# Kernel optimization log

Hardware: AMD Instinct MI355X
Metric: run time of the kernel (lower is better)

Reference implementation:

```python
import jax, jax.numpy as jnp
import numpy as np

N, E1, E2, P, H = 4096, 131072, 131072, 65536, 128
ROLE_VOCAB, ROLE_DIM, IDX_VOCAB, IDX_DIM = 8, 16, 1024, 8


def _lin_init(key, fan_in, fan_out):
    k1, k2 = jax.random.split(key)
    bound = 1.0 / np.sqrt(fan_in)
    W = jax.random.uniform(k1, (fan_in, fan_out), jnp.float32, -bound, bound)
    b = jax.random.uniform(k2, (fan_out,), jnp.float32, -bound, bound)
    return W, b


def setup_inputs() -> dict:
    key = jax.random.key(0)
    ks = jax.random.split(key, 24)
    d = {}
    d["block_features"] = jax.random.normal(ks[0], (N, 16), jnp.float32)
    d["role_ids"] = jax.random.randint(ks[1], (N,), 0, ROLE_VOCAB)
    d["b2b_src"] = jax.random.randint(ks[2], (E1,), 0, N)
    d["b2b_dst"] = jax.random.randint(ks[3], (E1,), 0, N)
    d["b2b_w"] = jax.random.uniform(ks[4], (E1,), jnp.float32)
    d["p2b_pin"] = jax.random.randint(ks[5], (E2,), 0, P)
    d["p2b_block"] = jax.random.randint(ks[6], (E2,), 0, N)
    d["p2b_w"] = jax.random.uniform(ks[7], (E2,), jnp.float32)
    d["pins_pos"] = jax.random.normal(ks[8], (P, 2), jnp.float32)
    d["area_targets"] = jax.random.uniform(ks[9], (N,), jnp.float32)
    # parameters
    d["role_emb"] = jax.random.normal(ks[10], (ROLE_VOCAB, ROLE_DIM), jnp.float32)
    d["idx_emb"] = jax.random.normal(ks[11], (IDX_VOCAB, IDX_DIM), jnp.float32)
    d["in_W1"], d["in_b1"] = _lin_init(ks[12], 16 + IDX_DIM + ROLE_DIM, H)
    d["in_W2"], d["in_b2"] = _lin_init(ks[13], H, H)
    d["b2b_W1"], d["b2b_b1"] = _lin_init(ks[14], 2 * H + 1, H)
    d["b2b_W2"], d["b2b_b2"] = _lin_init(ks[15], H, H)
    d["p2b_W1"], d["p2b_b1"] = _lin_init(ks[16], H + 3, H)
    d["p2b_W2"], d["p2b_b2"] = _lin_init(ks[17], H, H)
    d["self_W"], d["self_b"] = _lin_init(ks[18], H, H)
    d["ln_g"] = jnp.ones((H,), jnp.float32)
    d["ln_b"] = jnp.zeros((H,), jnp.float32)
    d["gp_W1"], d["gp_b1"] = _lin_init(ks[19], 2 * H, H)
    d["gp_W2"], d["gp_b2"] = _lin_init(ks[20], H, H)
    return d


def _mlp2(x, W1, b1, W2, b2):
    return jax.nn.relu(x @ W1 + b1) @ W2 + b2


def _forward(block_features, role_ids, b2b_src, b2b_dst, b2b_w, p2b_pin, p2b_block,
             p2b_w, pins_pos, area_targets, role_emb, idx_emb, in_W1, in_b1, in_W2,
             in_b2, b2b_W1, b2b_b1, b2b_W2, b2b_b2, p2b_W1, p2b_b1, p2b_W2, p2b_b2,
             self_W, self_b, ln_g, ln_b, gp_W1, gp_b1, gp_W2, gp_b2):
    n = block_features.shape[0]
    role_e = role_emb[role_ids]                       # [N, role_dim]
    idx_e = idx_emb[jnp.arange(n) % IDX_VOCAB]        # [N, idx_dim]
    x = jnp.concatenate([block_features, role_e, idx_e], axis=-1)
    h = jax.nn.relu(_mlp2(x, in_W1, in_b1, in_W2, in_b2))  # input_proj ends in ReLU

    # --- b2b messages: two directed messages per undirected edge ---
    max_b2b = jax.lax.stop_gradient(jnp.maximum(jnp.max(jnp.abs(b2b_w)), 1.0))
    w = (b2b_w / max_b2b)[:, None]                    # [E1, 1]
    hi, hj = h[b2b_src], h[b2b_dst]                   # [E1, H]
    m_ij = _mlp2(jnp.concatenate([hi, hj, w], -1), b2b_W1, b2b_b1, b2b_W2, b2b_b2)
    m_ji = _mlp2(jnp.concatenate([hj, hi, w], -1), b2b_W1, b2b_b1, b2b_W2, b2b_b2)
    agg = jnp.zeros_like(h).at[b2b_src].add(m_ij).at[b2b_dst].add(m_ji)

    # --- p2b messages ---
    total_area = jnp.maximum(jnp.sum(area_targets), 1e-6)
    case_scale = jax.lax.stop_gradient(jnp.maximum(jnp.sqrt(total_area), 1e-6))
    max_p2b = jax.lax.stop_gradient(jnp.maximum(jnp.max(jnp.abs(p2b_w)), 1.0))
    pin_feats = jnp.concatenate(
        [pins_pos[p2b_pin] / case_scale, (p2b_w / max_p2b)[:, None]], axis=-1)  # [E2, 3]
    m_p = _mlp2(jnp.concatenate([h[p2b_block], pin_feats], -1),
                p2b_W1, p2b_b1, p2b_W2, p2b_b2)
    agg = agg.at[p2b_block].add(m_p)

    # --- combine + LayerNorm ---
    z = h @ self_W + self_b + agg
    mu = jnp.mean(z, axis=-1, keepdims=True)
    var = jnp.mean(jnp.square(z - mu), axis=-1, keepdims=True)
    block_embeddings = (z - mu) / jnp.sqrt(var + 1e-5) * ln_g + ln_b

    pooled = jnp.concatenate(
        [block_embeddings.mean(axis=0), block_embeddings.max(axis=0)], axis=-1)
    graph_embedding = _mlp2(pooled, gp_W1, gp_b1, gp_W2, gp_b2)
    return block_embeddings, graph_embedding


def reference(block_features, role_ids, b2b_src, b2b_dst, b2b_w, p2b_pin, p2b_block,
              p2b_w, pins_pos, area_targets, role_emb, idx_emb, in_W1, in_b1, in_W2,
              in_b2, b2b_W1, b2b_b1, b2b_W2, b2b_b2, p2b_W1, p2b_b1, p2b_W2, p2b_b2,
              self_W, self_b, ln_g, ln_b, gp_W1, gp_b1, gp_W2, gp_b2):
    block_embeddings, graph_embedding = _forward(
        block_features, role_ids, b2b_src, b2b_dst, b2b_w, p2b_pin, p2b_block,
        p2b_w, pins_pos, area_targets, role_emb, idx_emb, in_W1, in_b1, in_W2,
        in_b2, b2b_W1, b2b_b1, b2b_W2, b2b_b2, p2b_W1, p2b_b1, p2b_W2, p2b_b2,
        self_W, self_b, ln_g, ln_b, gp_W1, gp_b1, gp_W2, gp_b2)
    block_mask = jnp.ones((block_features.shape[0],), dtype=bool)
    return block_embeddings, graph_embedding, block_mask
```

## Files before the change

### kernel.cpp

```cpp
#include <hip/hip_runtime.h>
#include <hip/hip_bf16.h>

#define N_NODES 4096
#define HDIM    128
#define E1      131072
#define E2      131072
#define NMSG_B2B (2 * E1)
#define CAPB    192
#define CAPP    96

#define OFF_PSUM   8
#define OFF_PMAX   136
#define OFF_HB     264
#define OFF_P      (OFF_HB + 262144)
#define OFF_Q      (OFF_P + 524288)
#define OFF_R      (OFF_Q + 524288)
#define OFF_CP     (OFF_R + 524288)
#define OFF_B2H    (OFF_CP + 24576)
#define OFF_B2L    (OFF_B2H + 8192)
#define OFF_P2H    (OFF_B2L + 8192)
#define OFF_P2L    (OFF_P2H + 8192)
#define OFF_SWP    (OFF_P2L + 8192)
#define OFF_IW1    (OFF_SWP + 8192)
#define OFF_IW2    (OFF_IW1 + 4096)
#define OFF_WLAST  (OFF_IW2 + 8192)
#define OFF_PEXTRA (OFF_WLAST + 128)
#define OFF_CNTB   (OFF_PEXTRA + 384)
#define OFF_CNTP   (OFF_CNTB + 4096)
#define OFF_BKB    (OFF_CNTP + 4096)
#define OFF_BKP    (OFF_BKB + 2 * N_NODES * CAPB)
#define WS_FLOATS  (OFF_BKP + 2 * N_NODES * CAPP)

typedef short short8 __attribute__((ext_vector_type(8)));
typedef float f32x4 __attribute__((ext_vector_type(4)));

__device__ __forceinline__ unsigned short f2bf(float f) {
  union { float f; unsigned u; } v; v.f = f;
  unsigned r = v.u + 0x7fffu + ((v.u >> 16) & 1u);
  return (unsigned short)(r >> 16);
}
__device__ __forceinline__ float bf2f(unsigned short h) {
  return __uint_as_float((unsigned)h << 16);
}
__device__ __forceinline__ int il(int c) { return ((c & 63) << 1) | (c >> 6); }

__global__ __launch_bounds__(256) void setup_kernel(const float* __restrict__ b2bw,
                                                    const float* __restrict__ p2bw,
                                                    const float* __restrict__ area,
                                                    const float* __restrict__ bW1,
                                                    const float* __restrict__ bW2,
                                                    const float* __restrict__ pW1,
                                                    const float* __restrict__ pW2,
                                                    const float* __restrict__ sWm,
                                                    const float* __restrict__ iW1,
                                                    const float* __restrict__ iW2,
                                                    float* __restrict__ ws) {
  __shared__ float red[256];
  int b = blockIdx.x, t = threadIdx.x;
  if (b < 32) {
    float m = 0.f;
    for (int i = b * 256 + t; i < E1; i += 32 * 256) m = fmaxf(m, fabsf(b2bw[i]));
    red[t] = m; __syncthreads();
    for (int s = 128; s > 0; s >>= 1) { if (t < s) red[t] = fmaxf(red[t], red[t + s]); __syncthreads(); }
    if (t == 0) atomicMax((unsigned*)&ws[0], __float_as_uint(red[0]));
  } else if (b < 64) {
    float m = 0.f;
    for (int i = (b - 32) * 256 + t; i < E2; i += 32 * 256) m = fmaxf(m, fabsf(p2bw[i]));
    red[t] = m; __syncthreads();
    for (int s = 128; s > 0; s >>= 1) { if (t < s) red[t] = fmaxf(red[t], red[t + s]); __syncthreads(); }
    if (t == 0) atomicMax((unsigned*)&ws[1], __float_as_uint(red[0]));
  } else if (b < 96) {
    float s0 = 0.f;
    for (int i = (b - 64) * 256 + t; i < N_NODES; i += 32 * 256) s0 += area[i];
    red[t] = s0; __syncthreads();
    for (int s = 128; s > 0; s >>= 1) { if (t < s) red[t] += red[t + s]; __syncthreads(); }
    if (t == 0) atomicAdd(&ws[2], red[0]);
  } else if (b == 96) {
    if (t < HDIM) ((int*)ws)[OFF_PMAX + t] = 0x80000000;
  } else {
    unsigned short* Cp  = (unsigned short*)(ws + OFF_CP);
    unsigned short* B2h = (unsigned short*)(ws + OFF_B2H);
    unsigned short* B2l = (unsigned short*)(ws + OFF_B2L);
    unsigned short* P2h = (unsigned short*)(ws + OFF_P2H);
    unsigned short* P2l = (unsigned short*)(ws + OFF_P2L);
    unsigned short* Swp = (unsigned short*)(ws + OFF_SWP);
    unsigned short* I1p = (unsigned short*)(ws + OFF_IW1);
    unsigned short* I2p = (unsigned short*)(ws + OFF_IW2);
    float* wlast = ws + OFF_WLAST;
    float* pextra = ws + OFF_PEXTRA;
    const int total = 156160;
    for (int x = (b - 97) * 256 + t; x < total; x += 128 * 256) {
      if (x < 49152) {
        int j = x & 7, lane = (x >> 3) & 63, ks = (x >> 9) & 3, nc = x >> 11;
        int col = nc * 16 + (lane & 15), k = ks * 32 + (lane >> 4) * 8 + j;
        float v;
        if (col < 128)      v = bW1[k * 128 + col];
        else if (col < 256) v = bW1[(128 + k) * 128 + (col - 128)];
        else                v = pW1[k * 128 + (col - 256)];
        Cp[x] = f2bf(v);
      } else if (x < 114688) {
        int u = (x - 49152) & 16383, which = (x - 49152) >> 14;
        int j = u & 7, lane = (u >> 3) & 63, ks = (u >> 9) & 3, nt = u >> 11;
        int n = nt * 16 + (lane & 15), k = ks * 32 + (lane >> 4) * 8 + j;
        float v = (which < 2) ? bW2[k * 128 + n] : pW2[k * 128 + n];
        unsigned short hi = f2bf(v);
        unsigned short outv = (which & 1) ? f2bf(v - bf2f(hi)) : hi;
        ((which < 2) ? ((which & 1) ? B2l : B2h) : ((which & 1) ? P2l : P2h))[u] = outv;
      } else if (x < 131072) {
        int u = x - 114688;
        int j = u & 7, lane = (u >> 3) & 63, ks = (u >> 9) & 3, nt = u >> 11;
        int n = nt * 16 + (lane & 15), k = ks * 32 + (lane >> 4) * 8 + j;
        Swp[u] = f2bf(sWm[k * 128 + n]);
      } else if (x < 139264) {
        int u = x - 131072;
        int j = u & 7, lane = (u >> 3) & 63, ks = (u >> 9) & 1, nt = u >> 10;
        int n = nt * 16 + (lane & 15), k = ks * 32 + (lane >> 4) * 8 + j;
        I1p[u] = (k < 40) ? f2bf(iW1[k * 128 + n]) : 0;
      } else if (x < 155648) {
        int u = x - 139264;
        int j = u & 7, lane = (u >> 3) & 63, ks = (u >> 9) & 3, nt = u >> 11;
        int n = nt * 16 + (lane & 15), k = ks * 32 + (lane >> 4) * 8 + j;
        I2p[u] = f2bf(iW2[k * 128 + n]);
      } else if (x < 155776) {
        int c = x - 155648;
        wlast[il(c)] = bW1[256 * 128 + c];
      } else {
        int u = x - 155776;
        int r = u >> 7, c = u & 127;
        pextra[r * 128 + il(c)] = pW1[(128 + r) * 128 + c];
      }
    }
  }
}

__global__ __launch_bounds__(512) void mid_kernel(const int* __restrict__ src,
                                                  const int* __restrict__ dst,
                                                  const int* __restrict__ pblk,
                                                  const int* __restrict__ ppin,
                                                  const float* __restrict__ bwv,
                                                  const float* __restrict__ pwv,
                                                  const float* __restrict__ pins,
                                                  const float* __restrict__ bfeat,
                                                  const int* __restrict__ rid,
                                                  const float* __restrict__ remb,
                                                  const float* __restrict__ iemb,
                                                  const float* __restrict__ ib1,
                                                  const float* __restrict__ ib2,
                                                  const float* __restrict__ bb1,
                                                  const float* __restrict__ pb1,
                                                  float* __restrict__ ws,
                                                  unsigned short* __restrict__ hb) {
  __shared__ __attribute__((aligned(16))) unsigned short xs[16 * 72];
  __shared__ __attribute__((aligned(16))) unsigned short h1s[16 * 136];
  __shared__ __attribute__((aligned(16))) unsigned short hs[16 * 136];
  int tid = threadIdx.x;
  if (blockIdx.x < 768) {
    int i = blockIdx.x * 512 + tid;
    int* cntB = (int*)ws + OFF_CNTB;
    int* cntP = (int*)ws + OFF_CNTP;
    uint2* BKB = (uint2*)((int*)ws + OFF_BKB);
    uint2* BKP = (uint2*)((int*)ws + OFF_BKP);
    if (i < NMSG_B2B) {
      int e = i >> 1, d = i & 1;
      int tg = d ? dst[e] : src[e];
      int o  = d ? src[e] : dst[e];
      int pos = atomicAdd(&cntB[tg], 1);
      if (pos < CAPB) {
        uint2 v; v.x = (unsigned)o; v.y = __float_as_uint(bwv[e]);
        BKB[tg * CAPB + pos] = v;
      }
    } else {
      int e = i - NMSG_B2B;
      int pin = ppin[e];
      int tg = pblk[e];
      int pos = atomicAdd(&cntP[tg], 1);
      if (pos < CAPP) {
        uint2 v;
        v.x = ((unsigned)f2bf(pins[pin * 2 + 1]) << 16) | (unsigned)f2bf(pins[pin * 2]);
        v.y = __float_as_uint(pwv[e]);
        BKP[tg * CAPP + pos] = v;
      }
    }
    return;
  }
  const unsigned short* I1p = (const unsigned short*)(ws + OFF_IW1);
  const unsigned short* I2p = (const unsigned short*)(ws + OFF_IW2);
  const unsigned short* Cp  = (const unsigned short*)(ws + OFF_CP);
  float* P = ws + OFF_P;
  float* Q = ws + OFF_Q;
  float* R = ws + OFF_R;
  int n0 = (blockIdx.x - 768) * 16;
  for (int idx = tid; idx < 1024; idx += 512) {
    int m = idx >> 6, c = idx & 63;
    int n = n0 + m;
    float v = 0.f;
    if (c < 16)      v = bfeat[n * 16 + c];
    else if (c < 32) v = remb[rid[n] * 16 + (c - 16)];
    else if (c < 40) v = iemb[(n & 1023) * 8 + (c - 32)];
    xs[m * 72 + c] = f2bf(v);
  }
  __syncthreads();
  int lane = tid & 63, wv = tid >> 6;
  int l15 = lane & 15, q = lane >> 4;
  f32x4 zero = {0.f, 0.f, 0.f, 0.f};
  f32x4 a1 = zero;
#pragma unroll
  for (int ks = 0; ks < 2; ks++) {
    short8 af = *(const short8*)(&xs[l15 * 72 + ks * 32 + q * 8]);
    short8 bfr = *(const short8*)(I1p + ((wv * 2 + ks) * 64 + lane) * 8);
    a1 = __builtin_amdgcn_mfma_f32_16x16x32_bf16(af, bfr, a1, 0, 0, 0);
  }
  {
    int n = wv * 16 + l15;
    float b = ib1[n];
#pragma unroll
    for (int r = 0; r < 4; r++)
      h1s[(q * 4 + r) * 136 + n] = f2bf(fmaxf(a1[r] + b, 0.f));
  }
  __syncthreads();
  f32x4 a2 = zero;
#pragma unroll
  for (int ks = 0; ks < 4; ks++) {
    short8 af = *(const short8*)(&h1s[l15 * 136 + ks * 32 + q * 8]);
    short8 bfr = *(const short8*)(I2p + ((wv * 4 + ks) * 64 + lane) * 8);
    a2 = __builtin_amdgcn_mfma_f32_16x16x32_bf16(af, bfr, a2, 0, 0, 0);
  }
  {
    int n = wv * 16 + l15;
    float b = ib2[n];
#pragma unroll
    for (int r = 0; r < 4; r++) {
      unsigned short hv = f2bf(fmaxf(a2[r] + b, 0.f));
      hs[(q * 4 + r) * 136 + n] = hv;
      hb[(n0 + q * 4 + r) * 128 + n] = hv;
    }
  }
  __syncthreads();
  f32x4 a3[3];
#pragma unroll
  for (int i = 0; i < 3; i++) a3[i] = zero;
#pragma unroll
  for (int ks = 0; ks < 4; ks++) {
    short8 af = *(const short8*)(&hs[l15 * 136 + ks * 32 + q * 8]);
#pragma unroll
    for (int j = 0; j < 3; j++) {
      short8 bfr = *(const short8*)(Cp + (((3 * wv + j) * 4 + ks) * 64 + lane) * 8);
      a3[j] = __builtin_amdgcn_mfma_f32_16x16x32_bf16(af, bfr, a3[j], 0, 0, 0);
    }
  }
#pragma unroll
  for (int j = 0; j < 3; j++) {
    int col = (3 * wv + j) * 16 + l15;
    int arr = col >> 7, cc = col & 127;
    float bias = (arr == 0) ? bb1[cc] : ((arr == 2) ? pb1[cc] : 0.f);
    float* dstp = (arr == 0) ? P : ((arr == 1) ? Q : R);
    int ic = il(cc);
#pragma unroll
    for (int r = 0; r < 4; r++)
      dstp[(n0 + q * 4 + r) * 128 + ic] = a3[j][r] + bias;
  }
}

__global__ __launch_bounds__(1024) void fused_kernel(const unsigned short* __restrict__ hb,
                                                     const float* __restrict__ sb,
                                                     const float* __restrict__ lng,
                                                     const float* __restrict__ lnb,
                                                     const float* __restrict__ bb2,
                                                     const float* __restrict__ pb2,
                                                     const float* __restrict__ gW1,
                                                     const float* __restrict__ gb1,
                                                     const float* __restrict__ gW2,
                                                     const float* __restrict__ gb2,
                                                     float* __restrict__ ws,
                                                     float* __restrict__ out) {
  __shared__ __attribute__((aligned(16))) unsigned short A[16 * 648];
  __shared__ float zp[2][16 * 128];
  __shared__ float zs[16 * 133];
  __shared__ float muS[16], rsg[16];
  __shared__ float partS[16][16], partQ[16][16];
  __shared__ float psumL[8][128];
  __shared__ int   pmaxL[8][128];
  __shared__ int   isLast;
  int tid = threadIdx.x;
  int n0 = blockIdx.x * 16;
  int lane = tid & 63, wv = tid >> 6;
  if (tid < 256) {
    int m = tid >> 4, o = (tid & 15) * 8;
    *(uint4*)(&A[m * 648 + o]) = *(const uint4*)(hb + (n0 + m) * 128 + o);
  }
  {
    const int* cntB = (const int*)ws + OFF_CNTB;
    const int* cntP = (const int*)ws + OFF_CNTP;
    const uint2* BKB = (const uint2*)((const int*)ws + OFF_BKB);
    const uint2* BKP = (const uint2*)((const int*)ws + OFF_BKP);
    const float* Pm = ws + OFF_P;
    const float* Qm = ws + OFF_Q;
    const float* Rm = ws + OFF_R;
    float invb = 1.f / fmaxf(__uint_as_float(((const unsigned*)ws)[0]), 1.f);
    float invp = 1.f / fmaxf(__uint_as_float(((const unsigned*)ws)[1]), 1.f);
    float cs = fmaxf(sqrtf(fmaxf(ws[2], 1e-6f)), 1e-6f);
    float invc = 1.f / cs;
    float2 wlr = *(const float2*)(ws + OFF_WLAST + 2 * lane);
    float2 e0r = *(const float2*)(ws + OFF_PEXTRA + 2 * lane);
    float2 e1r = *(const float2*)(ws + OFF_PEXTRA + 128 + 2 * lane);
    float2 e2r = *(const float2*)(ws + OFF_PEXTRA + 256 + 2 * lane);
    float2 wl = {invb * wlr.x, invb * wlr.y};
    float2 e0 = {invc * e0r.x, invc * e0r.y};
    float2 e1 = {invc * e1r.x, invc * e1r.y};
    float2 e2 = {invp * e2r.x, invp * e2r.y};
    int ln = wv;
    int node = n0 + ln;
    {
      int cnt = min(cntB[node], CAPB);
      const uint2* bk = BKB + node * CAPB;
      float2 p = *(const float2*)(Pm + node * 128 + 2 * lane);
      float a0 = 0.f, a1 = 0.f, b0 = 0.f, b1 = 0.f;
      int m = 0;
      for (; m + 8 <= cnt; m += 8) {
        uint2 k0 = bk[m],     k1 = bk[m + 1], k2 = bk[m + 2], k3 = bk[m + 3];
        uint2 k4 = bk[m + 4], k5 = bk[m + 5], k6 = bk[m + 6], k7 = bk[m + 7];
        float2 q0 = *(const float2*)(Qm + k0.x * 128 + 2 * lane);
        float2 q1 = *(const float2*)(Qm + k1.x * 128 + 2 * lane);
        float2 q2 = *(const float2*)(Qm + k2.x * 128 + 2 * lane);
        float2 q3 = *(const float2*)(Qm + k3.x * 128 + 2 * lane);
        float2 q4 = *(const float2*)(Qm + k4.x * 128 + 2 * lane);
        float2 q5 = *(const float2*)(Qm + k5.x * 128 + 2 * lane);
        float2 q6 = *(const float2*)(Qm + k6.x * 128 + 2 * lane);
        float2 q7 = *(const float2*)(Qm + k7.x * 128 + 2 * lane);
        float w0 = __uint_as_float(k0.y), w1 = __uint_as_float(k1.y);
        float w2 = __uint_as_float(k2.y), w3 = __uint_as_float(k3.y);
        float w4 = __uint_as_float(k4.y), w5 = __uint_as_float(k5.y);
        float w6 = __uint_as_float(k6.y), w7 = __uint_as_float(k7.y);
        a0 += fmaxf(fmaf(w0, wl.x, p.x) + q0.x, 0.f);
        a1 += fmaxf(fmaf(w0, wl.y, p.y) + q0.y, 0.f);
        b0 += fmaxf(fmaf(w1, wl.x, p.x) + q1.x, 0.f);
        b1 += fmaxf(fmaf(w1, wl.y, p.y) + q1.y, 0.f);
        a0 += fmaxf(fmaf(w2, wl.x, p.x) + q2.x, 0.f);
        a1 += fmaxf(fmaf(w2, wl.y, p.y) + q2.y, 0.f);
        b0 += fmaxf(fmaf(w3, wl.x, p.x) + q3.x, 0.f);
        b1 += fmaxf(fmaf(w3, wl.y, p.y) + q3.y, 0.f);
        a0 += fmaxf(fmaf(w4, wl.x, p.x) + q4.x, 0.f);
        a1 += fmaxf(fmaf(w4, wl.y, p.y) + q4.y, 0.f);
        b0 += fmaxf(fmaf(w5, wl.x, p.x) + q5.x, 0.f);
        b1 += fmaxf(fmaf(w5, wl.y, p.y) + q5.y, 0.f);
        a0 += fmaxf(fmaf(w6, wl.x, p.x) + q6.x, 0.f);
        a1 += fmaxf(fmaf(w6, wl.y, p.y) + q6.y, 0.f);
        b0 += fmaxf(fmaf(w7, wl.x, p.x) + q7.x, 0.f);
        b1 += fmaxf(fmaf(w7, wl.y, p.y) + q7.y, 0.f);
      }
      for (; m < cnt; m++) {
        uint2 k0 = bk[m];
        float w0 = __uint_as_float(k0.y);
        float2 q0 = *(const float2*)(Qm + k0.x * 128 + 2 * lane);
        a0 += fmaxf(fmaf(w0, wl.x, p.x) + q0.x, 0.f);
        a1 += fmaxf(fmaf(w0, wl.y, p.y) + q0.y, 0.f);
      }
      float s0 = a0 + b0;
      float s1 = a1 + b1;
      unsigned short h0 = f2bf(s0);
      A[ln * 648 + 128 + lane] = h0;
      A[ln * 648 + 256 + lane] = f2bf(s0 - bf2f(h0));
      unsigned short h1v = f2bf(s1);
      A[ln * 648 + 128 + 64 + lane] = h1v;
      A[ln * 648 + 256 + 64 + lane] = f2bf(s1 - bf2f(h1v));
    }
    {
      int cnt = min(cntP[node], CAPP);
      const uint2* bk = BKP + node * CAPP;
      float2 r = *(const float2*)(Rm + node * 128 + 2 * lane);
      float a0 = 0.f, a1 = 0.f, b0 = 0.f, b1 = 0.f;
      int m = 0;
      for (; m + 4 <= cnt; m += 4) {
        uint2 k0 = bk[m], k1 = bk[m + 1], k2 = bk[m + 2], k3 = bk[m + 3];
        float x00 = __uint_as_float((k0.x & 0xFFFFu) << 16);
        float x01 = __uint_as_float(k0.x & 0xFFFF0000u);
        float x02 = __uint_as_float(k0.y);
        float x10 = __uint_as_float((k1.x & 0xFFFFu) << 16);
        float x11 = __uint_as_float(k1.x & 0xFFFF0000u);
        float x12 = __uint_as_float(k1.y);
        float x20 = __uint_as_float((k2.x & 0xFFFFu) << 16);
        float x21 = __uint_as_float(k2.x & 0xFFFF0000u);
        float x22 = __uint_as_float(k2.y);
        float x30 = __uint_as_float((k3.x & 0xFFFFu) << 16);
        float x31 = __uint_as_float(k3.x & 0xFFFF0000u);
        float x32 = __uint_as_float(k3.y);
        a0 += fmaxf(fmaf(x02, e2.x, fmaf(x01, e1.x, fmaf(x00, e0.x, r.x))), 0.f);
        a1 += fmaxf(fmaf(x02, e2.y, fmaf(x01, e1.y, fmaf(x00, e0.y, r.y))), 0.f);
        b0 += fmaxf(fmaf(x12, e2.x, fmaf(x11, e1.x, fmaf(x10, e0.x, r.x))), 0.f);
        b1 += fmaxf(fmaf(x12, e2.y, fmaf(x11, e1.y, fmaf(x10, e0.y, r.y))), 0.f);
        a0 += fmaxf(fmaf(x22, e2.x, fmaf(x21, e1.x, fmaf(x20, e0.x, r.x))), 0.f);
        a1 += fmaxf(fmaf(x22, e2.y, fmaf(x21, e1.y, fmaf(x20, e0.y, r.y))), 0.f);
        b0 += fmaxf(fmaf(x32, e2.x, fmaf(x31, e1.x, fmaf(x30, e0.x, r.x))), 0.f);
        b1 += fmaxf(fmaf(x32, e2.y, fmaf(x31, e1.y, fmaf(x30, e0.y, r.y))), 0.f);
      }
      for (; m < cnt; m++) {
        uint2 k0 = bk[m];
        float x00 = __uint_as_float((k0.x & 0xFFFFu) << 16);
        float x01 = __uint_as_float(k0.x & 0xFFFF0000u);
        float x02 = __uint_as_float(k0.y);
        a0 += fmaxf(fmaf(x02, e2.x, fmaf(x01, e1.x, fmaf(x00, e0.x, r.x))), 0.f);
        a1 += fmaxf(fmaf(x02, e2.y, fmaf(x01, e1.y, fmaf(x00, e0.y, r.y))), 0.f);
      }
      float s0 = a0 + b0;
      float s1 = a1 + b1;
      unsigned short h0 = f2bf(s0);
      A[ln * 648 + 384 + lane] = h0;
      A[ln * 648 + 512 + lane] = f2bf(s0 - bf2f(h0));
      unsigned short h1v = f2bf(s1);
      A[ln * 648 + 384 + 64 + lane] = h1v;
      A[ln * 648 + 512 + 64 + lane] = f2bf(s1 - bf2f(h1v));
    }
  }
  __syncthreads();
  int l15 = lane & 15, q = lane >> 4;
  int ct = wv & 7, half = wv >> 3;
  f32x4 zero = {0.f, 0.f, 0.f, 0.f};
  f32x4 acc = zero;
  const unsigned short* bufs[7] = {
    (const unsigned short*)(ws + OFF_SWP), (const unsigned short*)(ws + OFF_B2H),
    (const unsigned short*)(ws + OFF_B2L), (const unsigned short*)(ws + OFF_B2H),
    (const unsigned short*)(ws + OFF_P2H), (const unsigned short*)(ws + OFF_P2L),
    (const unsigned short*)(ws + OFF_P2H)};
  const int segs[7] = {0, 128, 128, 256, 384, 384, 512};
  int p0 = half ? 4 : 0, p1 = half ? 7 : 4;
  for (int p = p0; p < p1; p++) {
#pragma unroll
    for (int ks = 0; ks < 4; ks++) {
      short8 af = *(const short8*)(&A[l15 * 648 + segs[p] + ks * 32 + q * 8]);
      short8 bfr = *(const short8*)(bufs[p] + ((ct * 4 + ks) * 64 + lane) * 8);
      acc = __builtin_amdgcn_mfma_f32_16x16x32_bf16(af, bfr, acc, 0, 0, 0);
    }
  }
  {
    int nn = ct * 16 + l15;
#pragma unroll
    for (int r = 0; r < 4; r++)
      zp[half][(q * 4 + r) * 128 + nn] = acc[r];
  }
  __syncthreads();
  const int* cntB = (const int*)ws + OFF_CNTB;
  const int* cntP = (const int*)ws + OFF_CNTP;
  {
    int idx = tid;
    for (int rep = 0; rep < 2; rep++, idx += 1024) {
      int row = idx >> 7, c = idx & 127;
      float cb = (float)cntB[n0 + row], cp = (float)cntP[n0 + row];
      zs[row * 133 + c] = zp[0][row * 128 + c] + zp[1][row * 128 + c]
                        + sb[c] + cb * bb2[c] + cp * pb2[c];
    }
  }
  __syncthreads();
  if (tid < 256) {
    int r = tid >> 4, g = tid & 15;
    const float* zr = &zs[r * 133 + g * 8];
    float s = 0.f, s2 = 0.f;
#pragma unroll
    for (int i = 0; i < 8; i++) { float v = zr[i]; s += v; s2 += v * v; }
    partS[r][g] = s; partQ[r][g] = s2;
  }
  __syncthreads();
  if (tid < 16) {
    float s = 0.f, s2 = 0.f;
#pragma unroll
    for (int g = 0; g < 16; g++) { s += partS[tid][g]; s2 += partQ[tid][g]; }
    float m = s * (1.f / 128.f);
    float var = s2 * (1.f / 128.f) - m * m;
    muS[tid] = m;
    rsg[tid] = rsqrtf(fmaxf(var, 0.f) + 1e-5f);
  }
  __syncthreads();
  {
    int c = tid & 127, grp = tid >> 7;
    float g = lng[c], b = lnb[c];
    float ls = 0.f; int lm = 0x80000000;
    for (int r = grp * 2; r < grp * 2 + 2; r++) {
      float v = (zs[r * 133 + c] - muS[r]) * rsg[r] * g + b;
      out[(n0 + r) * 128 + c] = v;
      ls += v;
      int e = __float_as_int(v);
      e = e >= 0 ? e : (e ^ 0x7fffffff);
      lm = max(lm, e);
    }
    psumL[grp][c] = ls; pmaxL[grp][c] = lm;
  }
  __syncthreads();
  if (tid < 128) {
    float s = 0.f; int mx = 0x80000000;
#pragma unroll
    for (int g = 0; g < 8; g++) { s += psumL[g][tid]; mx = max(mx, pmaxL[g][tid]); }
    atomicAdd(&ws[OFF_PSUM + tid], s);
    atomicMax(&((int*)ws)[OFF_PMAX + tid], mx);
  }
  if (tid < 16) out[N_NODES * HDIM + HDIM + n0 + tid] = 1.0f;
  __syncthreads();
  if (tid == 0) {
    __threadfence();
    int v = atomicAdd(&((int*)ws)[3], 1);
    isLast = (v == (int)gridDim.x - 1);
  }
  __syncthreads();
  if (!isLast) return;
  __shared__ float pooled[256];
  __shared__ float gpart[8][128];
  __shared__ float g1[128];
  if (tid < 128) {
    pooled[tid] = atomicAdd(&ws[OFF_PSUM + tid], 0.f) * (1.f / (float)N_NODES);
  } else if (tid < 256) {
    int e = atomicAdd(&((int*)ws)[OFF_PMAX + (tid - 128)], 0);
    int bits = e >= 0 ? e : (e ^ 0x7fffffff);
    pooled[tid] = __int_as_float(bits);
  }
  __syncthreads();
  {
    int c = tid & 127, g = tid >> 7;
    float acc2 = 0.f;
#pragma unroll 8
    for (int k = g * 32; k < g * 32 + 32; k++) acc2 += pooled[k] * gW1[k * 128 + c];
    gpart[g][c] = acc2;
  }
  __syncthreads();
  if (tid < 128) {
    float s = gb1[tid];
#pragma unroll
    for (int g = 0; g < 8; g++) s += gpart[g][tid];
    g1[tid] = fmaxf(s, 0.f);
  }
  __syncthreads();
  {
    int c = tid & 127, g = tid >> 7;
    float acc2 = 0.f;
#pragma unroll 8
    for (int k = g * 16; k < g * 16 + 16; k++) acc2 += g1[k] * gW2[k * 128 + c];
    gpart[g][c] = acc2;
  }
  __syncthreads();
  if (tid < 128) {
    float s = gb2[tid];
#pragma unroll
    for (int g = 0; g < 8; g++) s += gpart[g][tid];
    out[N_NODES * HDIM + tid] = s;
  }
}

extern "C" void kernel_launch(void* const* d_in, const int* in_sizes, int n_in,
                              void* d_out, int out_size, void* d_ws, size_t ws_size,
                              hipStream_t stream) {
  const float* bfeat = (const float*)d_in[0];
  const int*   rid   = (const int*)d_in[1];
  const int*   bsrc  = (const int*)d_in[2];
  const int*   bdst  = (const int*)d_in[3];
  const float* bw    = (const float*)d_in[4];
  const int*   ppin  = (const int*)d_in[5];
  const int*   pblk  = (const int*)d_in[6];
  const float* pw    = (const float*)d_in[7];
  const float* pins  = (const float*)d_in[8];
  const float* area  = (const float*)d_in[9];
  const float* remb  = (const float*)d_in[10];
  const float* iemb  = (const float*)d_in[11];
  const float* inW1  = (const float*)d_in[12];
  const float* inb1  = (const float*)d_in[13];
  const float* inW2  = (const float*)d_in[14];
  const float* inb2  = (const float*)d_in[15];
  const float* bW1   = (const float*)d_in[16];
  const float* bb1   = (const float*)d_in[17];
  const float* bW2   = (const float*)d_in[18];
  const float* bb2   = (const float*)d_in[19];
  const float* pW1   = (const float*)d_in[20];
  const float* pb1   = (const float*)d_in[21];
  const float* pW2   = (const float*)d_in[22];
  const float* pb2   = (const float*)d_in[23];
  const float* sW    = (const float*)d_in[24];
  const float* sb    = (const float*)d_in[25];
  const float* lng   = (const float*)d_in[26];
  const float* lnb   = (const float*)d_in[27];
  const float* gW1   = (const float*)d_in[28];
  const float* gb1   = (const float*)d_in[29];
  const float* gW2   = (const float*)d_in[30];
  const float* gb2   = (const float*)d_in[31];

  float* ws  = (float*)d_ws;
  float* out = (float*)d_out;
  unsigned short* hb = (unsigned short*)(ws + OFF_HB);
  int* cntB = (int*)ws + OFF_CNTB;

  hipMemsetAsync(d_ws, 0, 264 * sizeof(float), stream);
  hipMemsetAsync((void*)cntB, 0, 2 * 4096 * sizeof(int), stream);
  setup_kernel<<<225, 256, 0, stream>>>(bw, pw, area,
                                        bW1, bW2, pW1, pW2, sW, inW1, inW2, ws);
  mid_kernel<<<1024, 512, 0, stream>>>(bsrc, bdst, pblk, ppin, bw, pw, pins,
                                       bfeat, rid, remb, iemb, inb1, inb2, bb1, pb1,
                                       ws, hb);
  fused_kernel<<<256, 1024, 0, stream>>>(hb, sb, lng, lnb, bb2, pb2,
                                         gW1, gb1, gW2, gb2, ws, out);
}
```

Before: 195.6 us.

## Halve nodes per block and split each node's edge gather across two waves

The fused kernel now handles 8 nodes per block instead of 16 and launches 512 blocks. Each node's edge list is split between two wavefronts, and their partial sums are combined through shared memory before the bf16 hi/lo split. The MFMA A tile is zero-padded for the unused rows. Separately, the counter memset is folded into setup_kernel, removing one hipMemsetAsync launch. The aim is more parallelism and shorter per-wave gather chains, at the cost of half-wasted MFMA rows and an extra barrier.

```diff
diff --git a/kernel.cpp b/kernel.cpp
--- a/kernel.cpp
+++ b/kernel.cpp
@@ -77,6 +77,8 @@
     if (t == 0) atomicAdd(&ws[2], red[0]);
   } else if (b == 96) {
     if (t < HDIM) ((int*)ws)[OFF_PMAX + t] = 0x80000000;
+    int* cB = (int*)ws + OFF_CNTB;
+    for (int i = t; i < 2 * N_NODES; i += 256) cB[i] = 0;
   } else {
     unsigned short* Cp  = (unsigned short*)(ws + OFF_CP);
     unsigned short* B2h = (unsigned short*)(ws + OFF_B2H);
@@ -274,23 +276,29 @@
                                                      float* __restrict__ ws,
                                                      float* __restrict__ out) {
   __shared__ __attribute__((aligned(16))) unsigned short A[16 * 648];
-  __shared__ float zp[2][16 * 128];
-  __shared__ float zs[16 * 133];
-  __shared__ float muS[16], rsg[16];
-  __shared__ float partS[16][16], partQ[16][16];
+  __shared__ float partB[16][130];
+  __shared__ float partP[16][130];
+  __shared__ float zp[2][8 * 128];
+  __shared__ float zs[8 * 133];
+  __shared__ float muS[8], rsg[8];
+  __shared__ float partS[8][16], partQ[8][16];
   __shared__ float psumL[8][128];
   __shared__ int   pmaxL[8][128];
   __shared__ int   isLast;
   int tid = threadIdx.x;
-  int n0 = blockIdx.x * 16;
+  int n0 = blockIdx.x * 8;
   int lane = tid & 63, wv = tid >> 6;
-  if (tid < 256) {
+  const int* cntBp = (const int*)ws + OFF_CNTB;
+  const int* cntPp = (const int*)ws + OFF_CNTP;
+  if (tid < 128) {
     int m = tid >> 4, o = (tid & 15) * 8;
     *(uint4*)(&A[m * 648 + o]) = *(const uint4*)(hb + (n0 + m) * 128 + o);
   }
-  {
-    const int* cntB = (const int*)ws + OFF_CNTB;
-    const int* cntP = (const int*)ws + OFF_CNTP;
+  if (tid < 648) {
+    int r = tid / 81, o = (tid % 81) * 8;
+    *(uint4*)(&A[(8 + r) * 648 + o]) = make_uint4(0u, 0u, 0u, 0u);
+  }
+  {
     const uint2* BKB = (const uint2*)((const int*)ws + OFF_BKB);
     const uint2* BKP = (const uint2*)((const int*)ws + OFF_BKP);
     const float* Pm = ws + OFF_P;
@@ -308,15 +316,17 @@
     float2 e0 = {invc * e0r.x, invc * e0r.y};
     float2 e1 = {invc * e1r.x, invc * e1r.y};
     float2 e2 = {invp * e2r.x, invp * e2r.y};
-    int ln = wv;
+    int ln = wv >> 1, hf = wv & 1;
     int node = n0 + ln;
     {
-      int cnt = min(cntB[node], CAPB);
+      int cnt = min(cntBp[node], CAPB);
+      int mh = cnt >> 1;
+      int m = hf ? mh : 0;
+      int me = hf ? cnt : mh;
       const uint2* bk = BKB + node * CAPB;
       float2 p = *(const float2*)(Pm + node * 128 + 2 * lane);
       float a0 = 0.f, a1 = 0.f, b0 = 0.f, b1 = 0.f;
-      int m = 0;
-      for (; m + 8 <= cnt; m += 8) {
+      for (; m + 8 <= me; m += 8) {
         uint2 k0 = bk[m],     k1 = bk[m + 1], k2 = bk[m + 2], k3 = bk[m + 3];
         uint2 k4 = bk[m + 4], k5 = bk[m + 5], k6 = bk[m + 6], k7 = bk[m + 7];
         float2 q0 = *(const float2*)(Qm + k0.x * 128 + 2 * lane);
@@ -348,29 +358,25 @@
         b0 += fmaxf(fmaf(w7, wl.x, p.x) + q7.x, 0.f);
         b1 += fmaxf(fmaf(w7, wl.y, p.y) + q7.y, 0.f);
       }
-      for (; m < cnt; m++) {
+      for (; m < me; m++) {
         uint2 k0 = bk[m];
         float w0 = __uint_as_float(k0.y);
         float2 q0 = *(const float2*)(Qm + k0.x * 128 + 2 * lane);
         a0 += fmaxf(fmaf(w0, wl.x, p.x) + q0.x, 0.f);
         a1 += fmaxf(fmaf(w0, wl.y, p.y) + q0.y, 0.f);
       }
-      float s0 = a0 + b0;
-      float s1 = a1 + b1;
-      unsigned short h0 = f2bf(s0);
-      A[ln * 648 + 128 + lane] = h0;
-      A[ln * 648 + 256 + lane] = f2bf(s0 - bf2f(h0));
-      unsigned short h1v = f2bf(s1);
-      A[ln * 648 + 128 + 64 + lane] = h1v;
-      A[ln * 648 + 256 + 64 + lane] = f2bf(s1 - bf2f(h1v));
+      partB[wv][lane]      = a0 + b0;
+      partB[wv][64 + lane] = a1 + b1;
     }
     {
-      int cnt = min(cntP[node], CAPP);
+      int cnt = min(cntPp[node], CAPP);
+      int mh = cnt >> 1;
+      int m = hf ? mh : 0;
+      int me = hf ? cnt : mh;
       const uint2* bk = BKP + node * CAPP;
       float2 r = *(const float2*)(Rm + node * 128 + 2 * lane);
       float a0 = 0.f, a1 = 0.f, b0 = 0.f, b1 = 0.f;
-      int m = 0;
-      for (; m + 4 <= cnt; m += 4) {
+      for (; m + 4 <= me; m += 4) {
         uint2 k0 = bk[m], k1 = bk[m + 1], k2 = bk[m + 2], k3 = bk[m + 3];
         float x00 = __uint_as_float((k0.x & 0xFFFFu) << 16);
         float x01 = __uint_as_float(k0.x & 0xFFFF0000u);
@@ -393,7 +399,7 @@
         b0 += fmaxf(fmaf(x32, e2.x, fmaf(x31, e1.x, fmaf(x30, e0.x, r.x))), 0.f);
         b1 += fmaxf(fmaf(x32, e2.y, fmaf(x31, e1.y, fmaf(x30, e0.y, r.y))), 0.f);
       }
-      for (; m < cnt; m++) {
+      for (; m < me; m++) {
         uint2 k0 = bk[m];
         float x00 = __uint_as_float((k0.x & 0xFFFFu) << 16);
         float x01 = __uint_as_float(k0.x & 0xFFFF0000u);
@@ -401,15 +407,21 @@
         a0 += fmaxf(fmaf(x02, e2.x, fmaf(x01, e1.x, fmaf(x00, e0.x, r.x))), 0.f);
         a1 += fmaxf(fmaf(x02, e2.y, fmaf(x01, e1.y, fmaf(x00, e0.y, r.y))), 0.f);
       }
-      float s0 = a0 + b0;
-      float s1 = a1 + b1;
-      unsigned short h0 = f2bf(s0);
-      A[ln * 648 + 384 + lane] = h0;
-      A[ln * 648 + 512 + lane] = f2bf(s0 - bf2f(h0));
-      unsigned short h1v = f2bf(s1);
-      A[ln * 648 + 384 + 64 + lane] = h1v;
-      A[ln * 648 + 512 + 64 + lane] = f2bf(s1 - bf2f(h1v));
-    }
+      partP[wv][lane]      = a0 + b0;
+      partP[wv][64 + lane] = a1 + b1;
+    }
+  }
+  __syncthreads();
+  {
+    int r = tid >> 7, c = tid & 127;
+    float sb_ = partB[2 * r][c] + partB[2 * r + 1][c];
+    float sp_ = partP[2 * r][c] + partP[2 * r + 1][c];
+    unsigned short h0 = f2bf(sb_);
+    A[r * 648 + 128 + c] = h0;
+    A[r * 648 + 256 + c] = f2bf(sb_ - bf2f(h0));
+    unsigned short h1v = f2bf(sp_);
+    A[r * 648 + 384 + c] = h1v;
+    A[r * 648 + 512 + c] = f2bf(sp_ - bf2f(h1v));
   }
   __syncthreads();
   int l15 = lane & 15, q = lane >> 4;
@@ -431,26 +443,21 @@
       acc = __builtin_amdgcn_mfma_f32_16x16x32_bf16(af, bfr, acc, 0, 0, 0);
     }
   }
-  {
+  if (q < 2) {
     int nn = ct * 16 + l15;
 #pragma unroll
     for (int r = 0; r < 4; r++)
       zp[half][(q * 4 + r) * 128 + nn] = acc[r];
   }
   __syncthreads();
-  const int* cntB = (const int*)ws + OFF_CNTB;
-  const int* cntP = (const int*)ws + OFF_CNTP;
-  {
-    int idx = tid;
-    for (int rep = 0; rep < 2; rep++, idx += 1024) {
-      int row = idx >> 7, c = idx & 127;
-      float cb = (float)cntB[n0 + row], cp = (float)cntP[n0 + row];
-      zs[row * 133 + c] = zp[0][row * 128 + c] + zp[1][row * 128 + c]
-                        + sb[c] + cb * bb2[c] + cp * pb2[c];
-    }
-  }
-  __syncthreads();
-  if (tid < 256) {
+  {
+    int row = tid >> 7, c = tid & 127;
+    float cb = (float)cntBp[n0 + row], cp = (float)cntPp[n0 + row];
+    zs[row * 133 + c] = zp[0][row * 128 + c] + zp[1][row * 128 + c]
+                      + sb[c] + cb * bb2[c] + cp * pb2[c];
+  }
+  __syncthreads();
+  if (tid < 128) {
     int r = tid >> 4, g = tid & 15;
     const float* zr = &zs[r * 133 + g * 8];
     float s = 0.f, s2 = 0.f;
@@ -459,7 +466,7 @@
     partS[r][g] = s; partQ[r][g] = s2;
   }
   __syncthreads();
-  if (tid < 16) {
+  if (tid < 8) {
     float s = 0.f, s2 = 0.f;
 #pragma unroll
     for (int g = 0; g < 16; g++) { s += partS[tid][g]; s2 += partQ[tid][g]; }
@@ -470,18 +477,14 @@
   }
   __syncthreads();
   {
-    int c = tid & 127, grp = tid >> 7;
+    int row = tid >> 7, c = tid & 127;
     float g = lng[c], b = lnb[c];
-    float ls = 0.f; int lm = 0x80000000;
-    for (int r = grp * 2; r < grp * 2 + 2; r++) {
-      float v = (zs[r * 133 + c] - muS[r]) * rsg[r] * g + b;
-      out[(n0 + r) * 128 + c] = v;
-      ls += v;
-      int e = __float_as_int(v);
-      e = e >= 0 ? e : (e ^ 0x7fffffff);
-      lm = max(lm, e);
-    }
-    psumL[grp][c] = ls; pmaxL[grp][c] = lm;
+    float v = (zs[row * 133 + c] - muS[row]) * rsg[row] * g + b;
+    out[(n0 + row) * 128 + c] = v;
+    psumL[row][c] = v;
+    int e = __float_as_int(v);
+    e = e >= 0 ? e : (e ^ 0x7fffffff);
+    pmaxL[row][c] = e;
   }
   __syncthreads();
   if (tid < 128) {
@@ -491,7 +494,7 @@
     atomicAdd(&ws[OFF_PSUM + tid], s);
     atomicMax(&((int*)ws)[OFF_PMAX + tid], mx);
   }
-  if (tid < 16) out[N_NODES * HDIM + HDIM + n0 + tid] = 1.0f;
+  if (tid < 8) out[N_NODES * HDIM + HDIM + n0 + tid] = 1.0f;
   __syncthreads();
   if (tid == 0) {
     __threadfence();
@@ -581,15 +584,13 @@
   float* ws  = (float*)d_ws;
   float* out = (float*)d_out;
   unsigned short* hb = (unsigned short*)(ws + OFF_HB);
-  int* cntB = (int*)ws + OFF_CNTB;
 
   hipMemsetAsync(d_ws, 0, 264 * sizeof(float), stream);
-  hipMemsetAsync((void*)cntB, 0, 2 * 4096 * sizeof(int), stream);
   setup_kernel<<<225, 256, 0, stream>>>(bw, pw, area,
                                         bW1, bW2, pW1, pW2, sW, inW1, inW2, ws);
   mid_kernel<<<1024, 512, 0, stream>>>(bsrc, bdst, pblk, ppin, bw, pw, pins,
                                        bfeat, rid, remb, iemb, inb1, inb2, bb1, pb1,
                                        ws, hb);
-  fused_kernel<<<256, 1024, 0, stream>>>(hb, sb, lng, lnb, bb2, pb2,
+  fused_kernel<<<512, 1024, 0, stream>>>(hb, sb, lng, lnb, bb2, pb2,
                                          gW1, gb1, gW2, gb2, ws, out);
 }
```

Result: slower. 204.9 us (+4.7%).

## Halve nodes per block in fused kernel and fold count memset into setup

Applied to the files above, without the earlier changes.

The fused kernel now handles 8 nodes per 512-thread block (512 blocks) instead of 16 nodes per 1024-thread block. Each wave now runs the full 7-segment MFMA K loop on its own, so the split-K shared-memory reduction and one barrier go away; the unused 8 rows of the 16-row MFMA tile are zero-padded. The separate memset of the edge-count arrays is replaced by zeroing inside setup_kernel, which removes one launch. In exchange, half of each MFMA tile does wasted work and twice as many blocks contend on the global pooling atomics.

```diff
diff --git a/kernel.cpp b/kernel.cpp
--- a/kernel.cpp
+++ b/kernel.cpp
@@ -77,6 +77,8 @@
     if (t == 0) atomicAdd(&ws[2], red[0]);
   } else if (b == 96) {
     if (t < HDIM) ((int*)ws)[OFF_PMAX + t] = 0x80000000;
+    int* cB = (int*)ws + OFF_CNTB;
+    for (int i = t; i < 2 * N_NODES; i += 256) cB[i] = 0;
   } else {
     unsigned short* Cp  = (unsigned short*)(ws + OFF_CP);
     unsigned short* B2h = (unsigned short*)(ws + OFF_B2H);
@@ -261,36 +263,39 @@
   }
 }
 
-__global__ __launch_bounds__(1024) void fused_kernel(const unsigned short* __restrict__ hb,
-                                                     const float* __restrict__ sb,
-                                                     const float* __restrict__ lng,
-                                                     const float* __restrict__ lnb,
-                                                     const float* __restrict__ bb2,
-                                                     const float* __restrict__ pb2,
-                                                     const float* __restrict__ gW1,
-                                                     const float* __restrict__ gb1,
-                                                     const float* __restrict__ gW2,
-                                                     const float* __restrict__ gb2,
-                                                     float* __restrict__ ws,
-                                                     float* __restrict__ out) {
+__global__ __launch_bounds__(512) void fused_kernel(const unsigned short* __restrict__ hb,
+                                                    const float* __restrict__ sb,
+                                                    const float* __restrict__ lng,
+                                                    const float* __restrict__ lnb,
+                                                    const float* __restrict__ bb2,
+                                                    const float* __restrict__ pb2,
+                                                    const float* __restrict__ gW1,
+                                                    const float* __restrict__ gb1,
+                                                    const float* __restrict__ gW2,
+                                                    const float* __restrict__ gb2,
+                                                    float* __restrict__ ws,
+                                                    float* __restrict__ out) {
   __shared__ __attribute__((aligned(16))) unsigned short A[16 * 648];
-  __shared__ float zp[2][16 * 128];
-  __shared__ float zs[16 * 133];
-  __shared__ float muS[16], rsg[16];
-  __shared__ float partS[16][16], partQ[16][16];
+  __shared__ float zs[8 * 133];
+  __shared__ float muS[8], rsg[8];
+  __shared__ float partS[8][16], partQ[8][16];
   __shared__ float psumL[8][128];
   __shared__ int   pmaxL[8][128];
   __shared__ int   isLast;
   int tid = threadIdx.x;
-  int n0 = blockIdx.x * 16;
+  int n0 = blockIdx.x * 8;
   int lane = tid & 63, wv = tid >> 6;
-  if (tid < 256) {
+  const int* cntBp = (const int*)ws + OFF_CNTB;
+  const int* cntPp = (const int*)ws + OFF_CNTP;
+  if (tid < 128) {
     int m = tid >> 4, o = (tid & 15) * 8;
     *(uint4*)(&A[m * 648 + o]) = *(const uint4*)(hb + (n0 + m) * 128 + o);
   }
+  for (int i = tid; i < 648; i += 512) {
+    int r = i / 81, k = i - r * 81;
+    *(uint4*)(&A[(8 + r) * 648 + k * 8]) = make_uint4(0u, 0u, 0u, 0u);
+  }
   {
-    const int* cntB = (const int*)ws + OFF_CNTB;
-    const int* cntP = (const int*)ws + OFF_CNTP;
     const uint2* BKB = (const uint2*)((const int*)ws + OFF_BKB);
     const uint2* BKP = (const uint2*)((const int*)ws + OFF_BKP);
     const float* Pm = ws + OFF_P;
@@ -311,7 +316,7 @@
     int ln = wv;
     int node = n0 + ln;
     {
-      int cnt = min(cntB[node], CAPB);
+      int cnt = min(cntBp[node], CAPB);
       const uint2* bk = BKB + node * CAPB;
       float2 p = *(const float2*)(Pm + node * 128 + 2 * lane);
       float a0 = 0.f, a1 = 0.f, b0 = 0.f, b1 = 0.f;
@@ -365,7 +370,7 @@
       A[ln * 648 + 256 + 64 + lane] = f2bf(s1 - bf2f(h1v));
     }
     {
-      int cnt = min(cntP[node], CAPP);
+      int cnt = min(cntPp[node], CAPP);
       const uint2* bk = BKP + node * CAPP;
       float2 r = *(const float2*)(Rm + node * 128 + 2 * lane);
       float a0 = 0.f, a1 = 0.f, b0 = 0.f, b1 = 0.f;
@@ -413,7 +418,7 @@
   }
   __syncthreads();
   int l15 = lane & 15, q = lane >> 4;
-  int ct = wv & 7, half = wv >> 3;
+  int ct = wv;
   f32x4 zero = {0.f, 0.f, 0.f, 0.f};
   f32x4 acc = zero;
   const unsigned short* bufs[7] = {
@@ -422,8 +427,8 @@
     (const unsigned short*)(ws + OFF_P2H), (const unsigned short*)(ws + OFF_P2L),
     (const unsigned short*)(ws + OFF_P2H)};
   const int segs[7] = {0, 128, 128, 256, 384, 384, 512};
-  int p0 = half ? 4 : 0, p1 = half ? 7 : 4;
-  for (int p = p0; p < p1; p++) {
+#pragma unroll
+  for (int p = 0; p < 7; p++) {
 #pragma unroll
     for (int ks = 0; ks < 4; ks++) {
       short8 af = *(const short8*)(&A[l15 * 648 + segs[p] + ks * 32 + q * 8]);
@@ -431,26 +436,18 @@
       acc = __builtin_amdgcn_mfma_f32_16x16x32_bf16(af, bfr, acc, 0, 0, 0);
     }
   }
-  {
-    int nn = ct * 16 + l15;
-#pragma unroll
-    for (int r = 0; r < 4; r++)
-      zp[half][(q * 4 + r) * 128 + nn] = acc[r];
-  }
-  __syncthreads();
-  const int* cntB = (const int*)ws + OFF_CNTB;
-  const int* cntP = (const int*)ws + OFF_CNTP;
-  {
-    int idx = tid;
-    for (int rep = 0; rep < 2; rep++, idx += 1024) {
-      int row = idx >> 7, c = idx & 127;
-      float cb = (float)cntB[n0 + row], cp = (float)cntP[n0 + row];
-      zs[row * 133 + c] = zp[0][row * 128 + c] + zp[1][row * 128 + c]
-                        + sb[c] + cb * bb2[c] + cp * pb2[c];
-    }
-  }
-  __syncthreads();
-  if (tid < 256) {
+  if (q < 2) {
+    int col = ct * 16 + l15;
+    float sbv = sb[col], b2v = bb2[col], p2v = pb2[col];
+#pragma unroll
+    for (int r = 0; r < 4; r++) {
+      int row = q * 4 + r;
+      float cb = (float)cntBp[n0 + row], cp = (float)cntPp[n0 + row];
+      zs[row * 133 + col] = acc[r] + sbv + cb * b2v + cp * p2v;
+    }
+  }
+  __syncthreads();
+  if (tid < 128) {
     int r = tid >> 4, g = tid & 15;
     const float* zr = &zs[r * 133 + g * 8];
     float s = 0.f, s2 = 0.f;
@@ -459,7 +456,7 @@
     partS[r][g] = s; partQ[r][g] = s2;
   }
   __syncthreads();
-  if (tid < 16) {
+  if (tid < 8) {
     float s = 0.f, s2 = 0.f;
 #pragma unroll
     for (int g = 0; g < 16; g++) { s += partS[tid][g]; s2 += partQ[tid][g]; }
@@ -469,19 +466,16 @@
     rsg[tid] = rsqrtf(fmaxf(var, 0.f) + 1e-5f);
   }
   __syncthreads();
-  {
-    int c = tid & 127, grp = tid >> 7;
+  for (int rep = 0; rep < 2; rep++) {
+    int idx = tid + rep * 512;
+    int row = idx >> 7, c = idx & 127;
     float g = lng[c], b = lnb[c];
-    float ls = 0.f; int lm = 0x80000000;
-    for (int r = grp * 2; r < grp * 2 + 2; r++) {
-      float v = (zs[r * 133 + c] - muS[r]) * rsg[r] * g + b;
-      out[(n0 + r) * 128 + c] = v;
-      ls += v;
-      int e = __float_as_int(v);
-      e = e >= 0 ? e : (e ^ 0x7fffffff);
-      lm = max(lm, e);
-    }
-    psumL[grp][c] = ls; pmaxL[grp][c] = lm;
+    float v = (zs[row * 133 + c] - muS[row]) * rsg[row] * g + b;
+    out[(n0 + row) * 128 + c] = v;
+    psumL[row][c] = v;
+    int e = __float_as_int(v);
+    e = e >= 0 ? e : (e ^ 0x7fffffff);
+    pmaxL[row][c] = e;
   }
   __syncthreads();
   if (tid < 128) {
@@ -491,7 +485,7 @@
     atomicAdd(&ws[OFF_PSUM + tid], s);
     atomicMax(&((int*)ws)[OFF_PMAX + tid], mx);
   }
-  if (tid < 16) out[N_NODES * HDIM + HDIM + n0 + tid] = 1.0f;
+  if (tid < 8) out[N_NODES * HDIM + HDIM + n0 + tid] = 1.0f;
   __syncthreads();
   if (tid == 0) {
     __threadfence();
@@ -501,7 +495,7 @@
   __syncthreads();
   if (!isLast) return;
   __shared__ float pooled[256];
-  __shared__ float gpart[8][128];
+  __shared__ float gpart[4][128];
   __shared__ float g1[128];
   if (tid < 128) {
     pooled[tid] = atomicAdd(&ws[OFF_PSUM + tid], 0.f) * (1.f / (float)N_NODES);
@@ -515,14 +509,14 @@
     int c = tid & 127, g = tid >> 7;
     float acc2 = 0.f;
 #pragma unroll 8
-    for (int k = g * 32; k < g * 32 + 32; k++) acc2 += pooled[k] * gW1[k * 128 + c];
+    for (int k = g * 64; k < g * 64 + 64; k++) acc2 += pooled[k] * gW1[k * 128 + c];
     gpart[g][c] = acc2;
   }
   __syncthreads();
   if (tid < 128) {
     float s = gb1[tid];
 #pragma unroll
-    for (int g = 0; g < 8; g++) s += gpart[g][tid];
+    for (int g = 0; g < 4; g++) s += gpart[g][tid];
     g1[tid] = fmaxf(s, 0.f);
   }
   __syncthreads();
@@ -530,14 +524,14 @@
     int c = tid & 127, g = tid >> 7;
     float acc2 = 0.f;
 #pragma unroll 8
-    for (int k = g * 16; k < g * 16 + 16; k++) acc2 += g1[k] * gW2[k * 128 + c];
+    for (int k = g * 32; k < g * 32 + 32; k++) acc2 += g1[k] * gW2[k * 128 + c];
     gpart[g][c] = acc2;
   }
   __syncthreads();
   if (tid < 128) {
     float s = gb2[tid];
 #pragma unroll
-    for (int g = 0; g < 8; g++) s += gpart[g][tid];
+    for (int g = 0; g < 4; g++) s += gpart[g][tid];
     out[N_NODES * HDIM + tid] = s;
   }
 }
@@ -581,15 +575,13 @@
   float* ws  = (float*)d_ws;
   float* out = (float*)d_out;
   unsigned short* hb = (unsigned short*)(ws + OFF_HB);
-  int* cntB = (int*)ws + OFF_CNTB;
 
   hipMemsetAsync(d_ws, 0, 264 * sizeof(float), stream);
-  hipMemsetAsync((void*)cntB, 0, 2 * 4096 * sizeof(int), stream);
   setup_kernel<<<225, 256, 0, stream>>>(bw, pw, area,
                                         bW1, bW2, pW1, pW2, sW, inW1, inW2, ws);
   mid_kernel<<<1024, 512, 0, stream>>>(bsrc, bdst, pblk, ppin, bw, pw, pins,
                                        bfeat, rid, remb, iemb, inb1, inb2, bb1, pb1,
                                        ws, hb);
-  fused_kernel<<<256, 1024, 0, stream>>>(hb, sb, lng, lnb, bb2, pb2,
-                                         gW1, gb1, gW2, gb2, ws, out);
+  fused_kernel<<<512, 512, 0, stream>>>(hb, sb, lng, lnb, bb2, pb2,
+                                        gW1, gb1, gW2, gb2, ws, out);
 }
```

Result: no change. 198.1 us (+1.3%).
